# Kernel optimization log

Hardware: AMD Instinct MI355X
Metric: run time of the kernel (lower is better)

Reference implementation:

```python
import jax, jax.numpy as jnp
import numpy as np

B, T, D, H = 2, 2048, 1024, 16
DK = D // H
NEG = -1e9  # stand-in for -inf; causal mask guarantees >=1 valid key per row


def setup_inputs() -> dict:
    key = jax.random.key(0)
    ks = jax.random.split(key, 9)
    s = 1.0 / np.sqrt(D)
    x = jax.random.normal(ks[0], (B, T, D), dtype=jnp.float32)
    mask = jnp.broadcast_to(jnp.tril(jnp.ones((T, T), dtype=jnp.int32))[None, None], (B, 1, T, T))
    params = {}
    for i, n in enumerate(['q', 'k', 'v', 'o']):
        params['W' + n] = jax.random.normal(ks[1 + 2 * i], (D, D), dtype=jnp.float32) * s
        params['b' + n] = jax.random.normal(ks[2 + 2 * i], (D,), dtype=jnp.float32) * s
    return dict(x=x, mask=mask, **params)


def reference(x, mask, Wq, bq, Wk, bk, Wv, bv, Wo, bo):
    Bx, Tx, Dx = x.shape
    # projections: [B,T,D] -> [B,H,T,DK]
    def split_heads(y):
        return y.reshape(Bx, Tx, H, DK).transpose(0, 2, 1, 3)
    Q = split_heads(x @ Wq + bq)
    K = split_heads(x @ Wk + bk)
    V = split_heads(x @ Wv + bv)
    scores = jnp.einsum('bhqd,bhkd->bhqk', Q, K) / jnp.sqrt(jnp.float32(DK))
    scores = jnp.where(mask == 0, NEG, scores)
    attn = jax.nn.softmax(scores, axis=-1)  # dropout is identity in eval / p=0
    out = jnp.einsum('bhqk,bhkd->bhqd', attn, V)
    out = out.transpose(0, 2, 1, 3).reshape(Bx, Tx, Dx)
    return out @ Wo + bo
```

## Files before the change

kernel.cpp:

```cpp
#include <hip/hip_runtime.h>
#include <hip/hip_bf16.h>

typedef __bf16 bf16;
typedef __attribute__((ext_vector_type(8))) __bf16 bf16x8;
typedef __attribute__((ext_vector_type(4))) __bf16 bf16x4;
typedef __attribute__((ext_vector_type(4))) float f32x4;

#define TSEQ 2048
#define DMODEL 1024
#define NHEAD 16
#define DKH 64
#define BATCH 2
#define NQKV 3072

typedef __attribute__((address_space(1))) const void gv_t;
typedef __attribute__((address_space(3))) void sv_t;
__device__ __forceinline__ void gll16(const bf16* g, bf16* s) {
    __builtin_amdgcn_global_load_lds((gv_t*)g, (sv_t*)s, 16, 0, 0);
}
#define WAIT_VM(n) __builtin_amdgcn_s_waitcnt(0x0F70 | (n))

#define PREP_CONV 4096
#define PREP_TW   4096
#define PREP_GRID (PREP_CONV + PREP_TW + 12)
__global__ __launch_bounds__(256) void prep(
    const float* __restrict__ x,
    const float* __restrict__ Wq, const float* __restrict__ Wk,
    const float* __restrict__ Wv, const float* __restrict__ Wo,
    const float* __restrict__ bq, const float* __restrict__ bk,
    const float* __restrict__ bv,
    bf16* __restrict__ xb, bf16* __restrict__ WT, float* __restrict__ biasO)
{
    __shared__ float t[32][33];
    int bid = blockIdx.x;
    const int tid = threadIdx.x;
    if (bid < PREP_CONV) {
        int i = (bid * 256 + tid) * 4;
        f32x4 v = *(const f32x4*)(x + i);
        bf16x4 o;
#pragma unroll
        for (int j = 0; j < 4; ++j) o[j] = (bf16)v[j];
        *(bf16x4*)(xb + i) = o;
        return;
    }
    bid -= PREP_CONV;
    if (bid < PREP_TW) {
        int z = bid >> 10;
        int by = ((bid >> 5) & 31) * 32, bx = (bid & 31) * 32;
        const float* W = z == 0 ? Wq : z == 1 ? Wk : z == 2 ? Wv : Wo;
        bf16* T = WT + (size_t)z * DMODEL * DMODEL;
        int tx = tid & 31, ty = tid >> 5;
#pragma unroll
        for (int i = 0; i < 4; ++i)
            t[ty + i * 8][tx] = W[(size_t)(by + ty + i * 8) * DMODEL + bx + tx];
        __syncthreads();
#pragma unroll
        for (int i = 0; i < 4; ++i)
            T[(size_t)(bx + ty + i * 8) * DMODEL + by + tx] = (bf16)t[tx][ty + i * 8];
        return;
    }
    bid -= PREP_TW;
    int i = bid * 256 + tid;
    float v = i < 1024 ? bq[i] : i < 2048 ? bk[i - 1024] : bv[i - 2048];
    biasO[i] = v;
}

template <typename OutT, int NW_N, bool FUSE_VT>
__global__ __launch_bounds__(256) void gemm_bias_kernel(
    const bf16* __restrict__ A, const bf16* __restrict__ BT,
    const float* __restrict__ bias, OutT* __restrict__ C, int ldc,
    bf16* __restrict__ VT)
{
    constexpr int BN    = NW_N * 64;
    constexpr int MW    = 4 / NW_N;
    constexpr int WROWS = 128 / MW;
    constexpr int FM    = WROWS / 16;
    constexpr int ASZ   = 128 * 32;
    constexpr int BSZ   = BN * 32;
    constexpr int BNP   = BN + 4;
    constexpr int TST   = 136;
    constexpr int EPI   = sizeof(OutT) == 2 ? (FUSE_VT ? 128 * TST : 128 * BN)
                                            : 64 * BNP * 2;
    constexpr int STG   = 2 * ASZ + 2 * BSZ;
    constexpr int SMEM  = STG > EPI ? STG : EPI;
    __shared__ bf16 smem[SMEM];
    bf16* As0 = smem;
    bf16* Bs0 = smem + 2 * ASZ;

    const int tid = threadIdx.x;
    const int ln = tid & 63, wave = tid >> 6;
    const int wm = NW_N == 2 ? (wave >> 1) : wave;
    const int wn = NW_N == 2 ? (wave & 1) : 0;
    const int lr = ln & 15, quad = ln >> 4;
    const int m0 = blockIdx.y * 128, n0 = blockIdx.x * BN;

    f32x4 acc[FM][4] = {};

    const int grow = ln >> 2;
    const int gcol = (ln & 3) * 8;
    const bf16* Ag = A + (size_t)(m0 + wave * 32 + grow) * DMODEL + gcol;
    const bf16* Bg = BT + (size_t)(n0 + (NW_N == 2 ? wave * 32 : wave * 16) + grow) * DMODEL + gcol;

    auto stage = [&](int buf, int kk) {
        bf16* AsW = As0 + buf * ASZ + wave * 1024;
        gll16(Ag + kk, AsW);
        gll16(Ag + (size_t)16 * DMODEL + kk, AsW + 512);
        if constexpr (NW_N == 2) {
            bf16* BsW = Bs0 + buf * BSZ + wave * 1024;
            gll16(Bg + kk, BsW);
            gll16(Bg + (size_t)16 * DMODEL + kk, BsW + 512);
        } else {
            gll16(Bg + kk, Bs0 + buf * BSZ + wave * 512);
        }
    };

    constexpr int NT = DMODEL / 32;
    stage(0, 0);
    WAIT_VM(0);
    __syncthreads();
    for (int kt = 0; kt < NT; ++kt) {
        if (kt + 1 < NT) stage((kt + 1) & 1, (kt + 1) * 32);
        const bf16* AsB = As0 + (kt & 1) * ASZ;
        const bf16* BsB = Bs0 + (kt & 1) * BSZ;
        bf16x8 af[FM], bfr[4];
#pragma unroll
        for (int i = 0; i < FM; ++i)
            af[i] = *(const bf16x8*)(AsB + (wm * WROWS + i * 16 + lr) * 32 + quad * 8);
#pragma unroll
        for (int j = 0; j < 4; ++j)
            bfr[j] = *(const bf16x8*)(BsB + (wn * 64 + j * 16 + lr) * 32 + quad * 8);
#pragma unroll
        for (int i = 0; i < FM; ++i)
#pragma unroll
            for (int j = 0; j < 4; ++j)
                acc[i][j] = __builtin_amdgcn_mfma_f32_16x16x32_bf16(
                    af[i], bfr[j], acc[i][j], 0, 0, 0);
        WAIT_VM(0);
        __syncthreads();
    }

    if constexpr (sizeof(OutT) == 2) {
        if (FUSE_VT && n0 >= 2048) {
            bf16* Cs = smem;
#pragma unroll
            for (int j = 0; j < 4; ++j) {
                int nl = wn * 64 + j * 16 + lr;
                float bv = bias[n0 + nl];
#pragma unroll
                for (int i = 0; i < FM; ++i) {
                    int ml = wm * WROWS + i * 16 + quad * 4;
#pragma unroll
                    for (int r = 0; r < 4; ++r)
                        Cs[nl * TST + ml + r] = (bf16)(acc[i][j][r] + bv);
                }
            }
            __syncthreads();
            const int bb = m0 >> 11;
            const int tloc = m0 & 2047;
#pragma unroll
            for (int p = 0; p < 8; ++p) {
                int dl = p * 16 + (tid >> 4);
                int t0 = (tid & 15) * 8;
                bf16x8 v = *(const bf16x8*)(Cs + dl * TST + t0);
                *(bf16x8*)(VT + (size_t)(bb * 1024 + (n0 - 2048) + dl) * TSEQ +
                           tloc + t0) = v;
            }
            return;
        }
        bf16* Cs = smem;
#pragma unroll
        for (int j = 0; j < 4; ++j) {
            int nl = wn * 64 + j * 16 + lr;
            float bv = bias[n0 + nl];
#pragma unroll
            for (int i = 0; i < FM; ++i) {
                int ml = wm * WROWS + i * 16 + quad * 4;
#pragma unroll
                for (int r = 0; r < 4; ++r)
                    Cs[(ml + r) * BN + nl] = (bf16)(acc[i][j][r] + bv);
            }
        }
        __syncthreads();
        constexpr int LPR = BN / 8;
        constexpr int RPP = 256 / LPR;
        const int rr = tid / LPR, cc = (tid % LPR) * 8;
#pragma unroll
        for (int p = 0; p < 128 / RPP; ++p) {
            int row = p * RPP + rr;
            *(bf16x8*)(C + (size_t)(m0 + row) * ldc + n0 + cc) =
                *(const bf16x8*)(Cs + row * BN + cc);
        }
    } else {
        float* Cf = (float*)smem;
#pragma unroll
        for (int half = 0; half < 2; ++half) {
            if (((wm * WROWS) >> 6) == half) {
#pragma unroll
                for (int j = 0; j < 4; ++j) {
                    int nl = wn * 64 + j * 16 + lr;
                    float bv = bias[n0 + nl];
#pragma unroll
                    for (int i = 0; i < FM; ++i) {
                        int ml = wm * WROWS + i * 16 + quad * 4 - half * 64;
#pragma unroll
                        for (int r = 0; r < 4; ++r)
                            Cf[(ml + r) * BNP + nl] = acc[i][j][r] + bv;
                    }
                }
            }
            __syncthreads();
            constexpr int LPR = BN / 4;
            constexpr int RPP = 256 / LPR;
            const int rr = tid / LPR, cc = (tid % LPR) * 4;
#pragma unroll
            for (int p = 0; p < 64 / RPP; ++p) {
                int row = p * RPP + rr;
                *(f32x4*)(C + (size_t)(m0 + half * 64 + row) * ldc + n0 + cc) =
                    *(const f32x4*)(Cf + row * BNP + cc);
            }
            __syncthreads();
        }
    }
}

template <bool MASK>
__device__ __forceinline__ float softmax_store(
    const f32x4 st[4], bf16* __restrict__ Pw,
    int qrow, int kc, int lr, int quad, int sw)
{
    const float scale2 = 0.18033688f;
    float rs = 0.f;
#pragma unroll
    for (int kt = 0; kt < 4; ++kt) {
        bf16x4 p4;
#pragma unroll
        for (int r = 0; r < 4; ++r) {
            float p = exp2f(fmaf(st[kt][r], scale2, -24.0f));
            if (MASK && (kc + kt * 16 + quad * 4 + r > qrow)) p = 0.f;
            rs += p;
            p4[r] = (bf16)p;
        }
        *(bf16x4*)(Pw + lr * 64 + (((kt * 2 + (quad >> 1)) ^ sw) * 8) +
                   (quad & 1) * 4) = p4;
    }
    rs += __shfl_xor(rs, 16);
    rs += __shfl_xor(rs, 32);
    return rs;
}

template <int MODE>
__device__ __forceinline__ void attn_chunk(
    int kc, int qA, int qB, int lr, int quad,
    const bf16* __restrict__ KsB, const bf16* __restrict__ VsB,
    bf16* __restrict__ PwA, bf16* __restrict__ PwB,
    const bf16x8 qbA[2], const bf16x8 qbB[2],
    f32x4 oA[4], f32x4 oB[4], float& lA, float& lB)
{
    constexpr bool TWO = (MODE < 2);
    const int sw = lr & 7;
    bf16x8 kb[4][2];
#pragma unroll
    for (int kt = 0; kt < 4; ++kt)
#pragma unroll
        for (int kk = 0; kk < 2; ++kk)
            kb[kt][kk] = *(const bf16x8*)(KsB + (kt * 16 + lr) * 64 +
                                          (((kk * 4 + quad) ^ sw) * 8));
    f32x4 stB[4] = {};
#pragma unroll
    for (int kt = 0; kt < 4; ++kt)
#pragma unroll
        for (int kk = 0; kk < 2; ++kk)
            stB[kt] = __builtin_amdgcn_mfma_f32_16x16x32_bf16(
                kb[kt][kk], qbB[kk], stB[kt], 0, 0, 0);
    f32x4 stA[4] = {};
    if constexpr (TWO) {
#pragma unroll
        for (int kt = 0; kt < 4; ++kt)
#pragma unroll
            for (int kk = 0; kk < 2; ++kk)
                stA[kt] = __builtin_amdgcn_mfma_f32_16x16x32_bf16(
                    kb[kt][kk], qbA[kk], stA[kt], 0, 0, 0);
    }

    lB += softmax_store<MODE == 3>(stB, PwB, qB, kc, lr, quad, sw);
    if constexpr (TWO)
        lA += softmax_store<MODE == 1>(stA, PwA, qA, kc, lr, quad, sw);

#pragma unroll
    for (int kk = 0; kk < 2; ++kk) {
        bf16x8 pb = *(const bf16x8*)(PwB + lr * 64 + (((kk * 4 + quad) ^ sw) * 8));
        bf16x8 pa;
        if constexpr (TWO)
            pa = *(const bf16x8*)(PwA + lr * 64 + (((kk * 4 + quad) ^ sw) * 8));
#pragma unroll
        for (int dt = 0; dt < 4; ++dt) {
            bf16x8 vb = *(const bf16x8*)(VsB + (dt * 16 + lr) * 64 +
                                         (((kk * 4 + quad) ^ sw) * 8));
            oB[dt] = __builtin_amdgcn_mfma_f32_16x16x32_bf16(
                pb, vb, oB[dt], 0, 0, 0);
            if constexpr (TWO)
                oA[dt] = __builtin_amdgcn_mfma_f32_16x16x32_bf16(
                    pa, vb, oA[dt], 0, 0, 0);
        }
    }
}

__global__ __launch_bounds__(256, 2) void flash_attn(
    const bf16* __restrict__ QKV, const bf16* __restrict__ VT,
    bf16* __restrict__ O)
{
    __shared__ bf16 Ks[2][64 * 64];
    __shared__ bf16 Vs[2][64 * 64];
    __shared__ bf16 Pl[8][16 * 64];
    const int tid = threadIdx.x;
    const int ln = tid & 63, w = tid >> 6;
    const int lr = ln & 15, quad = ln >> 4;
    const int wg = blockIdx.x;
    const int g = wg & 31, p = wg >> 5;
    const int h = g >> 1, b = g & 1;
    const int xbA = p, xbB = 31 - p;
    const int q0A = xbA * 64, q0B = xbB * 64;
    const int qA = q0A + w * 16 + lr, qB = q0B + w * 16 + lr;
    bf16* PwA = Pl[w];
    bf16* PwB = Pl[4 + w];

    const bf16* Qb = QKV + (size_t)b * TSEQ * NQKV + h * DKH;
    const bf16* Kb = Qb + 1024;
    const bf16* VTb = VT + (size_t)(b * NHEAD + h) * DKH * TSEQ;

    const int srow = (w & 1) * 32 + (ln >> 3);
    const int scol = ((ln & 7) ^ ((ln >> 3) & 7)) * 8;
    const bool stK = (w < 2);

    auto stage = [&](int buf, int kc) {
        if (stK) {
            const bf16* g2 = Kb + (size_t)(kc + srow) * NQKV + scol;
            bf16* s = &Ks[buf][(w & 1) * 32 * 64];
#pragma unroll
            for (int l = 0; l < 4; ++l)
                gll16(g2 + (size_t)(l * 8) * NQKV, s + l * 8 * 64);
        } else {
            const bf16* g2 = VTb + (size_t)srow * TSEQ + kc + scol;
            bf16* s = &Vs[buf][(w & 1) * 32 * 64];
#pragma unroll
            for (int l = 0; l < 4; ++l)
                gll16(g2 + (size_t)(l * 8) * TSEQ, s + l * 8 * 64);
        }
    };

    bf16x8 qbA[2], qbB[2];
#pragma unroll
    for (int kk = 0; kk < 2; ++kk) {
        qbA[kk] = *(const bf16x8*)(Qb + (size_t)qA * NQKV + kk * 32 + quad * 8);
        qbB[kk] = *(const bf16x8*)(Qb + (size_t)qB * NQKV + kk * 32 + quad * 8);
    }
    WAIT_VM(0);

    f32x4 oA[4] = {}, oB[4] = {};
    float lA = 0.f, lB = 0.f;

    const int nld = xbB + 1;
    stage(0, 0);
    WAIT_VM(0);
    __syncthreads();
    for (int c = 0; c < nld; ++c) {
        if (c + 1 < nld) stage((c + 1) & 1, (c + 1) * 64);
        const int kc = c * 64;
        const bf16* K = Ks[c & 1];
        const bf16* V = Vs[c & 1];
        if (c < xbA)
            attn_chunk<0>(kc, qA, qB, lr, quad, K, V, PwA, PwB, qbA, qbB, oA, oB, lA, lB);
        else if (c == xbA)
            attn_chunk<1>(kc, qA, qB, lr, quad, K, V, PwA, PwB, qbA, qbB, oA, oB, lA, lB);
        else if (c == nld - 1)
            attn_chunk<3>(kc, qA, qB, lr, quad, K, V, PwA, PwB, qbA, qbB, oA, oB, lA, lB);
        else
            attn_chunk<2>(kc, qA, qB, lr, quad, K, V, PwA, PwB, qbA, qbB, oA, oB, lA, lB);
        WAIT_VM(0);
        __syncthreads();
    }

#pragma unroll
    for (int r = 0; r < 4; ++r) {
        float invB = 1.0f / __shfl(lB, quad * 4 + r);
        int rowB = q0B + w * 16 + quad * 4 + r;
#pragma unroll
        for (int dt = 0; dt < 4; ++dt)
            O[(size_t)(b * TSEQ + rowB) * DMODEL + h * DKH + dt * 16 + lr] =
                (bf16)(oB[dt][r] * invB);
    }
#pragma unroll
    for (int r = 0; r < 4; ++r) {
        float invA = 1.0f / __shfl(lA, quad * 4 + r);
        int rowA = q0A + w * 16 + quad * 4 + r;
#pragma unroll
        for (int dt = 0; dt < 4; ++dt)
            O[(size_t)(b * TSEQ + rowA) * DMODEL + h * DKH + dt * 16 + lr] =
                (bf16)(oA[dt][r] * invA);
    }
}

extern "C" void kernel_launch(void* const* d_in, const int* in_sizes, int n_in,
                              void* d_out, int out_size, void* d_ws, size_t ws_size,
                              hipStream_t stream)
{
    const float* x  = (const float*)d_in[0];
    const float* Wq = (const float*)d_in[2];
    const float* bq = (const float*)d_in[3];
    const float* Wk = (const float*)d_in[4];
    const float* bk = (const float*)d_in[5];
    const float* Wv = (const float*)d_in[6];
    const float* bv = (const float*)d_in[7];
    const float* Wo = (const float*)d_in[8];
    const float* bo = (const float*)d_in[9];

    char* ws = (char*)d_ws;
    bf16* xb   = (bf16*)(ws);
    bf16* QKV  = (bf16*)(ws + (8u  << 20));
    bf16* VT   = (bf16*)(ws + (32u << 20));
    bf16* O    = (bf16*)(ws + (40u << 20));
    bf16* WT   = (bf16*)(ws + (48u << 20));
    float* wsBias = (float*)O;

    prep<<<PREP_GRID, 256, 0, stream>>>(x, Wq, Wk, Wv, Wo, bq, bk, bv,
                                        xb, WT, wsBias);

    gemm_bias_kernel<bf16, 2, true><<<dim3(NQKV / 128, 32), 256, 0, stream>>>(
        xb, WT, wsBias, QKV, NQKV, VT);

    flash_attn<<<512, 256, 0, stream>>>(QKV, VT, O);

    gemm_bias_kernel<float, 1, false><<<dim3(DMODEL / 64, 32), 256, 0, stream>>>(
        O, WT + 3u * (1u << 20), bo, (float*)d_out, DMODEL, nullptr);
}
```

Measured before the change: 208.4 us.

## Switch attention to 32x32x16 MFMA with register-resident P and split-K waves

Result: no change. 209.1 us (+0.3%).

```diff
diff --git a/kernel.cpp b/kernel.cpp
--- a/kernel.cpp
+++ b/kernel.cpp
@@ -5,6 +5,8 @@
 typedef __attribute__((ext_vector_type(8))) __bf16 bf16x8;
 typedef __attribute__((ext_vector_type(4))) __bf16 bf16x4;
 typedef __attribute__((ext_vector_type(4))) float f32x4;
+typedef __attribute__((ext_vector_type(16))) float f32x16;
+typedef __attribute__((ext_vector_type(4))) int int4v;
 
 #define TSEQ 2048
 #define DMODEL 1024
@@ -19,6 +21,12 @@
     __builtin_amdgcn_global_load_lds((gv_t*)g, (sv_t*)s, 16, 0, 0);
 }
 #define WAIT_VM(n) __builtin_amdgcn_s_waitcnt(0x0F70 | (n))
+
+__device__ __forceinline__ unsigned cvtpk(float lo, float hi) {
+    unsigned d;
+    asm("v_cvt_pk_bf16_f32 %0, %1, %2" : "=v"(d) : "v"(lo), "v"(hi));
+    return d;
+}
 
 #define PREP_CONV 4096
 #define PREP_TW   4096
@@ -223,86 +231,62 @@
     }
 }
 
-template <bool MASK>
-__device__ __forceinline__ float softmax_store(
-    const f32x4 st[4], bf16* __restrict__ Pw,
-    int qrow, int kc, int lr, int quad, int sw)
+template <int KTN, bool MASKED>
+__device__ __forceinline__ void tile_step(
+    int kt0, int kc, int qabs,
+    const bf16* __restrict__ Ksb, const bf16* __restrict__ Vsb,
+    const bf16x8 qf[4], f32x16 oacc[2], float& lrow,
+    int ln31, int hi, int sw)
 {
+    f32x16 st[KTN] = {};
+#pragma unroll
+    for (int t = 0; t < KTN; ++t)
+#pragma unroll
+        for (int ks = 0; ks < 4; ++ks) {
+            const bf16x8 ka = *(const bf16x8*)(
+                Ksb + (ln31 + (kt0 + t) * 32) * 64 + (((2 * ks + hi) ^ sw) * 8));
+            st[t] = __builtin_amdgcn_mfma_f32_32x32x16_bf16(ka, qf[ks], st[t], 0, 0, 0);
+        }
+
     const float scale2 = 0.18033688f;
     float rs = 0.f;
 #pragma unroll
-    for (int kt = 0; kt < 4; ++kt) {
-        bf16x4 p4;
-#pragma unroll
-        for (int r = 0; r < 4; ++r) {
-            float p = exp2f(fmaf(st[kt][r], scale2, -24.0f));
-            if (MASK && (kc + kt * 16 + quad * 4 + r > qrow)) p = 0.f;
+    for (int t = 0; t < KTN; ++t)
+#pragma unroll
+        for (int r = 0; r < 16; ++r) {
+            float p = exp2f(fmaf(st[t][r], scale2, -24.0f));
+            if (MASKED &&
+                (kc + (kt0 + t) * 32 + (r & 3) + 8 * (r >> 2) + 4 * hi > qabs))
+                p = 0.f;
             rs += p;
-            p4[r] = (bf16)p;
-        }
-        *(bf16x4*)(Pw + lr * 64 + (((kt * 2 + (quad >> 1)) ^ sw) * 8) +
-                   (quad & 1) * 4) = p4;
-    }
-    rs += __shfl_xor(rs, 16);
+            st[t][r] = p;
+        }
     rs += __shfl_xor(rs, 32);
-    return rs;
-}
-
-template <int MODE>
-__device__ __forceinline__ void attn_chunk(
-    int kc, int qA, int qB, int lr, int quad,
-    const bf16* __restrict__ KsB, const bf16* __restrict__ VsB,
-    bf16* __restrict__ PwA, bf16* __restrict__ PwB,
-    const bf16x8 qbA[2], const bf16x8 qbB[2],
-    f32x4 oA[4], f32x4 oB[4], float& lA, float& lB)
-{
-    constexpr bool TWO = (MODE < 2);
-    const int sw = lr & 7;
-    bf16x8 kb[4][2];
-#pragma unroll
-    for (int kt = 0; kt < 4; ++kt)
-#pragma unroll
-        for (int kk = 0; kk < 2; ++kk)
-            kb[kt][kk] = *(const bf16x8*)(KsB + (kt * 16 + lr) * 64 +
-                                          (((kk * 4 + quad) ^ sw) * 8));
-    f32x4 stB[4] = {};
-#pragma unroll
-    for (int kt = 0; kt < 4; ++kt)
-#pragma unroll
-        for (int kk = 0; kk < 2; ++kk)
-            stB[kt] = __builtin_amdgcn_mfma_f32_16x16x32_bf16(
-                kb[kt][kk], qbB[kk], stB[kt], 0, 0, 0);
-    f32x4 stA[4] = {};
-    if constexpr (TWO) {
-#pragma unroll
-        for (int kt = 0; kt < 4; ++kt)
-#pragma unroll
-            for (int kk = 0; kk < 2; ++kk)
-                stA[kt] = __builtin_amdgcn_mfma_f32_16x16x32_bf16(
-                    kb[kt][kk], qbA[kk], stA[kt], 0, 0, 0);
-    }
-
-    lB += softmax_store<MODE == 3>(stB, PwB, qB, kc, lr, quad, sw);
-    if constexpr (TWO)
-        lA += softmax_store<MODE == 1>(stA, PwA, qA, kc, lr, quad, sw);
-
-#pragma unroll
-    for (int kk = 0; kk < 2; ++kk) {
-        bf16x8 pb = *(const bf16x8*)(PwB + lr * 64 + (((kk * 4 + quad) ^ sw) * 8));
-        bf16x8 pa;
-        if constexpr (TWO)
-            pa = *(const bf16x8*)(PwA + lr * 64 + (((kk * 4 + quad) ^ sw) * 8));
-#pragma unroll
-        for (int dt = 0; dt < 4; ++dt) {
-            bf16x8 vb = *(const bf16x8*)(VsB + (dt * 16 + lr) * 64 +
-                                         (((kk * 4 + quad) ^ sw) * 8));
-            oB[dt] = __builtin_amdgcn_mfma_f32_16x16x32_bf16(
-                pb, vb, oB[dt], 0, 0, 0);
-            if constexpr (TWO)
-                oA[dt] = __builtin_amdgcn_mfma_f32_16x16x32_bf16(
-                    pa, vb, oA[dt], 0, 0, 0);
-        }
-    }
+    lrow += rs;
+
+#pragma unroll
+    for (int t = 0; t < KTN; ++t)
+#pragma unroll
+        for (int s2 = 0; s2 < 2; ++s2) {
+            const int bb = s2 * 8;
+            unsigned c01 = cvtpk(st[t][bb + 0], st[t][bb + 1]);
+            unsigned c23 = cvtpk(st[t][bb + 2], st[t][bb + 3]);
+            unsigned c45 = cvtpk(st[t][bb + 4], st[t][bb + 5]);
+            unsigned c67 = cvtpk(st[t][bb + 6], st[t][bb + 7]);
+            asm("v_permlane32_swap_b32 %0, %1" : "+v"(c01), "+v"(c45));
+            asm("v_permlane32_swap_b32 %0, %1" : "+v"(c23), "+v"(c67));
+            int4v pw;
+            pw[0] = (int)c01; pw[1] = (int)c23; pw[2] = (int)c45; pw[3] = (int)c67;
+            const bf16x8 pa = __builtin_bit_cast(bf16x8, pw);
+            const int ksg = (kt0 + t) * 2 + s2;
+#pragma unroll
+            for (int dblk = 0; dblk < 2; ++dblk) {
+                const bf16x8 vb = *(const bf16x8*)(
+                    Vsb + (dblk * 32 + ln31) * 64 + (((2 * ksg + hi) ^ sw) * 8));
+                oacc[dblk] = __builtin_amdgcn_mfma_f32_32x32x16_bf16(
+                    pa, vb, oacc[dblk], 0, 0, 0);
+            }
+        }
 }
 
 __global__ __launch_bounds__(256, 2) void flash_attn(
@@ -311,27 +295,32 @@
 {
     __shared__ bf16 Ks[2][64 * 64];
     __shared__ bf16 Vs[2][64 * 64];
-    __shared__ bf16 Pl[8][16 * 64];
     const int tid = threadIdx.x;
     const int ln = tid & 63, w = tid >> 6;
-    const int lr = ln & 15, quad = ln >> 4;
+    const int ln31 = ln & 31, hi = ln >> 5, sw = ln & 7;
     const int wg = blockIdx.x;
     const int g = wg & 31, p = wg >> 5;
     const int h = g >> 1, b = g & 1;
-    const int xbA = p, xbB = 31 - p;
-    const int q0A = xbA * 64, q0B = xbB * 64;
-    const int qA = q0A + w * 16 + lr, qB = q0B + w * 16 + lr;
-    bf16* PwA = Pl[w];
-    bf16* PwB = Pl[4 + w];
+    const int q0A = p * 64, q0B = (31 - p) * 64;
 
     const bf16* Qb = QKV + (size_t)b * TSEQ * NQKV + h * DKH;
     const bf16* Kb = Qb + 1024;
     const bf16* VTb = VT + (size_t)(b * NHEAD + h) * DKH * TSEQ;
 
+    const int q1 = (w < 2 ? q0A : q0B) + (w & 1) * 32 + ln31;
+    const int q2 = q0B + (w & 1) * 32 + ln31;
+
+    bf16x8 qf1[4], qf2[4];
+#pragma unroll
+    for (int ks = 0; ks < 4; ++ks) {
+        qf1[ks] = *(const bf16x8*)(Qb + (size_t)q1 * NQKV + ks * 16 + hi * 8);
+        qf2[ks] = *(const bf16x8*)(Qb + (size_t)q2 * NQKV + ks * 16 + hi * 8);
+    }
+    WAIT_VM(0);
+
     const int srow = (w & 1) * 32 + (ln >> 3);
     const int scol = ((ln & 7) ^ ((ln >> 3) & 7)) * 8;
     const bool stK = (w < 2);
-
     auto stage = [&](int buf, int kc) {
         if (stK) {
             const bf16* g2 = Kb + (size_t)(kc + srow) * NQKV + scol;
@@ -348,18 +337,10 @@
         }
     };
 
-    bf16x8 qbA[2], qbB[2];
-#pragma unroll
-    for (int kk = 0; kk < 2; ++kk) {
-        qbA[kk] = *(const bf16x8*)(Qb + (size_t)qA * NQKV + kk * 32 + quad * 8);
-        qbB[kk] = *(const bf16x8*)(Qb + (size_t)qB * NQKV + kk * 32 + quad * 8);
-    }
-    WAIT_VM(0);
-
-    f32x4 oA[4] = {}, oB[4] = {};
-    float lA = 0.f, lB = 0.f;
-
-    const int nld = xbB + 1;
+    f32x16 oacc1[2] = {}, oacc2[2] = {};
+    float l1 = 0.f, l2 = 0.f;
+
+    const int nld = 32 - p;
     stage(0, 0);
     WAIT_VM(0);
     __syncthreads();
@@ -368,35 +349,67 @@
         const int kc = c * 64;
         const bf16* K = Ks[c & 1];
         const bf16* V = Vs[c & 1];
-        if (c < xbA)
-            attn_chunk<0>(kc, qA, qB, lr, quad, K, V, PwA, PwB, qbA, qbB, oA, oB, lA, lB);
-        else if (c == xbA)
-            attn_chunk<1>(kc, qA, qB, lr, quad, K, V, PwA, PwB, qbA, qbB, oA, oB, lA, lB);
-        else if (c == nld - 1)
-            attn_chunk<3>(kc, qA, qB, lr, quad, K, V, PwA, PwB, qbA, qbB, oA, oB, lA, lB);
-        else
-            attn_chunk<2>(kc, qA, qB, lr, quad, K, V, PwA, PwB, qbA, qbB, oA, oB, lA, lB);
+        if (c <= p) {
+            if (w < 2 && c == p)
+                tile_step<2, true >(0, kc, q1, K, V, qf1, oacc1, l1, ln31, hi, sw);
+            else
+                tile_step<2, false>(0, kc, q1, K, V, qf1, oacc1, l1, ln31, hi, sw);
+        } else {
+            const int kt0 = w >> 1;
+            if (c == nld - 1)
+                tile_step<1, true >(kt0, kc, q2, K, V, qf2, oacc2, l2, ln31, hi, sw);
+            else
+                tile_step<1, false>(kt0, kc, q2, K, V, qf2, oacc2, l2, ln31, hi, sw);
+        }
         WAIT_VM(0);
         __syncthreads();
     }
 
-#pragma unroll
-    for (int r = 0; r < 4; ++r) {
-        float invB = 1.0f / __shfl(lB, quad * 4 + r);
-        int rowB = q0B + w * 16 + quad * 4 + r;
-#pragma unroll
-        for (int dt = 0; dt < 4; ++dt)
-            O[(size_t)(b * TSEQ + rowB) * DMODEL + h * DKH + dt * 16 + lr] =
-                (bf16)(oB[dt][r] * invB);
-    }
-#pragma unroll
-    for (int r = 0; r < 4; ++r) {
-        float invA = 1.0f / __shfl(lA, quad * 4 + r);
-        int rowA = q0A + w * 16 + quad * 4 + r;
-#pragma unroll
-        for (int dt = 0; dt < 4; ++dt)
-            O[(size_t)(b * TSEQ + rowA) * DMODEL + h * DKH + dt * 16 + lr] =
-                (bf16)(oA[dt][r] * invA);
+    float* exO = (float*)&Ks[0][0];
+    float* exL = (float*)&Vs[0][0];
+    if (w < 2) {
+        float* dst = exO + w * 2048;
+#pragma unroll
+        for (int dblk = 0; dblk < 2; ++dblk)
+#pragma unroll
+            for (int r = 0; r < 16; ++r) {
+                int q = (r & 3) + 8 * (r >> 2) + 4 * hi;
+                dst[q * 64 + dblk * 32 + ln31] = oacc2[dblk][r];
+            }
+        if (ln < 32) exL[w * 32 + ln] = l2;
+    }
+    __syncthreads();
+
+    f32x16 oat[2];
+    float lt;
+    int qs;
+    if (w < 2) {
+        oat[0] = oacc1[0]; oat[1] = oacc1[1];
+        lt = l1;
+        qs = q0A + (w & 1) * 32;
+    } else {
+        const float* src = exO + (w - 2) * 2048;
+        lt = l1 + l2 + exL[(w - 2) * 32 + ln31];
+#pragma unroll
+        for (int dblk = 0; dblk < 2; ++dblk)
+#pragma unroll
+            for (int r = 0; r < 16; ++r) {
+                int q = (r & 3) + 8 * (r >> 2) + 4 * hi;
+                oat[dblk][r] = oacc1[dblk][r] + oacc2[dblk][r] +
+                               src[q * 64 + dblk * 32 + ln31];
+            }
+        qs = q0B + (w & 1) * 32;
+    }
+
+#pragma unroll
+    for (int r = 0; r < 16; ++r) {
+        const int crow = (r & 3) + 8 * (r >> 2) + 4 * hi;
+        const float inv = 1.0f / __shfl(lt, crow);
+        const int row = qs + crow;
+#pragma unroll
+        for (int dblk = 0; dblk < 2; ++dblk)
+            O[(size_t)(b * TSEQ + row) * DMODEL + h * DKH + dblk * 32 + ln31] =
+                (bf16)(oat[dblk][r] * inv);
     }
 }
 
```
